# Optimization experiments

Measured on AMD Instinct MI355X. Metric: run time of the kernel, lower is better.

Reference implementation:

```python
import jax, jax.numpy as jnp
import numpy as np

B, L, D, H, WIN, EXP = 2, 4096, 1024, 16, 256, 4

def setup_inputs() -> dict:
    key = jax.random.key(0)
    ks = jax.random.split(key, 8)
    F = EXP * D
    p = lambda k, shape: jax.random.normal(k, shape, dtype=jnp.float32) * 0.02
    return {
        "x": jax.random.normal(ks[0], (B, L, D), dtype=jnp.float32),
        "mask": jnp.zeros((B, L), dtype=jnp.float32),  # 0 = local attention everywhere
        "Wq": p(ks[1], (D, D)), "bq": jnp.zeros((D,), jnp.float32),
        "Wk": p(ks[2], (D, D)), "bk": jnp.zeros((D,), jnp.float32),
        "Wv": p(ks[3], (D, D)), "bv": jnp.zeros((D,), jnp.float32),
        "ln_g": jnp.ones((D,), jnp.float32), "ln_b": jnp.zeros((D,), jnp.float32),
        "W1": p(ks[4], (D, F)), "b1": jnp.zeros((F,), jnp.float32),
        "W2": p(ks[5], (F, D)), "b2": jnp.zeros((D,), jnp.float32),
    }


def reference(x, mask, Wq, bq, Wk, bk, Wv, bv, ln_g, ln_b, W1, b1, W2, b2):
    NEG = jnp.asarray(-1e9, x.dtype)
    Bs, Ls, Ds = x.shape
    dh = Ds // H
    c = WIN // 2  # one-sided window size (HF uses attention_window // 2)
    pad = WIN - Ls % WIN
    xp = jnp.pad(x, ((0, 0), (0, pad), (0, 0)))  # pad_token_id == 0
    mp = jnp.pad(mask, ((0, 0), (0, pad)), constant_values=-10000.0)
    S = Ls + pad
    n = S // c  # number of query chunks of size c

    inv_sqrt_dh = jnp.asarray(1.0 / np.sqrt(dh), x.dtype)
    q = ((xp @ Wq + bq) * inv_sqrt_dh).reshape(Bs, S, H, dh)
    k = (xp @ Wk + bk).reshape(Bs, S, H, dh)
    v = (xp @ Wv + bv).reshape(Bs, S, H, dh)

    # pad keys/values by one chunk on each side so query chunk i sees chunks i-1,i,i+1
    kp = jnp.pad(k, ((0, 0), (c, c), (0, 0), (0, 0)))
    vp = jnp.pad(v, ((0, 0), (c, c), (0, 0), (0, 0)))
    kvalid = jnp.pad(mp == 0.0, ((0, 0), (c, c)), constant_values=False)  # [B, S+2c]

    idx = jnp.arange(n)[:, None] * c + jnp.arange(3 * c)[None, :]  # [n, 3c]
    kc = kp[:, idx]   # [B, n, 3c, H, dh]
    vc = vp[:, idx]   # [B, n, 3c, H, dh]
    kvc = kvalid[:, idx]  # [B, n, 3c]
    qc = q.reshape(Bs, n, c, H, dh)

    scores = jnp.einsum('bnphd,bnrhd->bhnpr', qc, kc)  # [B,H,n,c,3c]
    p_ = jnp.arange(c)[:, None]
    r_ = jnp.arange(3 * c)[None, :]
    band = (r_ >= p_) & (r_ <= p_ + 2 * c)  # exact |i-j| <= c band, [c,3c]
    valid = band[None, None, None, :, :] & kvc[:, None, :, None, :]
    scores = jnp.where(valid, scores, NEG)
    probs = jax.nn.softmax(scores, axis=-1)
    attn = jnp.einsum('bhnpr,bnrhd->bnphd', probs, vc).reshape(Bs, S, Ds)

    h = (xp + attn)[:, :Ls]  # residual then drop padding (matches module order)
    mu = jnp.mean(h, axis=-1, keepdims=True)
    var = jnp.var(h, axis=-1, keepdims=True)
    h = (h - mu) / jnp.sqrt(var + 1e-5) * ln_g + ln_b
    out = h + (jax.nn.gelu(h @ W1 + b1, approximate=False) @ W2 + b2)
    return out
```

## Files before the change

### kernel.cpp

```cpp
#include <hip/hip_runtime.h>
#include <hip/hip_bf16.h>
#include <cstdint>

typedef __attribute__((ext_vector_type(8))) short short8;
typedef __attribute__((ext_vector_type(4))) short short4v;
typedef __attribute__((ext_vector_type(4))) float floatx4;

constexpr int B_ = 2, L_ = 4096, D_ = 1024, H_ = 16, DH = 64, F_ = 4096;
constexpr int M_ = B_ * L_;
constexpr int NQKV = 3 * D_;
constexpr int VT_GUARD = 512;

constexpr size_t OFF_XB  = 0;
constexpr size_t OFF_WCT = OFF_XB  + (size_t)M_ * D_ * 2;
constexpr size_t OFF_W1T = OFF_WCT + (size_t)NQKV * D_ * 2;
constexpr size_t OFF_W2T = OFF_W1T + (size_t)F_ * D_ * 2;
constexpr size_t OFF_QKV = OFF_W2T + (size_t)D_ * F_ * 2;
constexpr size_t OFF_VT  = OFF_QKV + (size_t)M_ * NQKV * 2;
constexpr size_t OFF_ATT = OFF_VT  + ((size_t)B_*H_*DH*L_ + 2*VT_GUARD) * 2;
constexpr size_t OFF_HB  = OFF_ATT + (size_t)M_ * D_ * 2;
constexpr size_t OFF_MID = OFF_HB  + (size_t)M_ * D_ * 2;

static __device__ __forceinline__ float b2f(unsigned short u) {
    union { unsigned int i; float f; } v; v.i = ((unsigned int)u) << 16; return v.f;
}

static __device__ __forceinline__ void gload16(const void* g, void* l) {
    __builtin_amdgcn_global_load_lds(
        (const __attribute__((address_space(1))) uint32_t*)g,
        (__attribute__((address_space(3))) uint32_t*)l, 16, 0, 0);
}

__global__ __launch_bounds__(256) void k_cvt_x(const float* __restrict__ x,
                                               __hip_bfloat16* __restrict__ xb) {
    int i = (blockIdx.x * 256 + threadIdx.x) * 8;
    float4 a = *(const float4*)(x + i);
    float4 b = *(const float4*)(x + i + 4);
    alignas(16) __hip_bfloat16 t[8];
    t[0] = __float2bfloat16(a.x); t[1] = __float2bfloat16(a.y);
    t[2] = __float2bfloat16(a.z); t[3] = __float2bfloat16(a.w);
    t[4] = __float2bfloat16(b.x); t[5] = __float2bfloat16(b.y);
    t[6] = __float2bfloat16(b.z); t[7] = __float2bfloat16(b.w);
    *(uint4*)(xb + i) = *(const uint4*)t;
}

__global__ __launch_bounds__(256) void k_tcvt(const float* __restrict__ in,
                                              __hip_bfloat16* __restrict__ out,
                                              int R, int C) {
    __shared__ float t[64][65];
    int tx = threadIdx.x & 63, ty4 = threadIdx.x >> 6;
    int c0 = blockIdx.x * 64, r0 = blockIdx.y * 64;
#pragma unroll
    for (int i = 0; i < 16; i++) {
        int r = ty4 + i * 4;
        t[r][tx] = in[(size_t)(r0 + r) * C + c0 + tx];
    }
    __syncthreads();
#pragma unroll
    for (int i = 0; i < 16; i++) {
        int r = ty4 + i * 4;
        out[(size_t)(c0 + r) * R + r0 + tx] = __float2bfloat16(t[tx][r]);
    }
}

__global__ __launch_bounds__(256) void k_vtrans(const __hip_bfloat16* __restrict__ qkv,
                                                __hip_bfloat16* __restrict__ vtg) {
    __shared__ __hip_bfloat16 t[64][72];
    int tx = threadIdx.x & 63, ty4 = threadIdx.x >> 6;
    int bh = blockIdx.y, b = bh >> 4, h = bh & 15;
    int j0 = blockIdx.x * 64;
#pragma unroll
    for (int i = 0; i < 16; i++) {
        int j = ty4 + i * 4;
        t[j][tx] = qkv[(size_t)(b * L_ + j0 + j) * NQKV + 2 * D_ + h * DH + tx];
    }
    __syncthreads();
#pragma unroll
    for (int i = 0; i < 16; i++) {
        int d = ty4 + i * 4;
        vtg[(long)(bh * DH + d) * L_ + j0 + tx] = t[tx][d];
    }
}

template<int NBN, int GM, int EPI, int KTOT>
__global__ __launch_bounds__(256, 2)
void k_g2(const __hip_bfloat16* __restrict__ A, const __hip_bfloat16* __restrict__ BT,
          const float* __restrict__ b0p, const float* __restrict__ b1p,
          const float* __restrict__ b2p,
          __hip_bfloat16* __restrict__ obf, float* __restrict__ of32,
          const __hip_bfloat16* __restrict__ hres) {
    constexpr int KT = KTOT / 64;
    constexpr int NTOT = NBN * 128;
    constexpr int PER = GM * NBN;
    __shared__ __hip_bfloat16 As[2 * 2 * 128 * 32];
    __shared__ __hip_bfloat16 Bs[2 * 2 * 128 * 32];

    const int tid = threadIdx.x, wave = tid >> 6, lane = tid & 63;
    const int lo = lane & 15, hi = lane >> 4;
    const int wm = wave >> 1, wn = wave & 1;

    const int nwg = gridDim.x, q = nwg >> 3;
    const int bid = blockIdx.x;
    const int swz = (bid & 7) * q + (bid >> 3);
    const int g = swz / PER, r = swz % PER;
    const int bm = g * GM + (r % GM);
    const int bn = r / GM;
    const size_t m0 = (size_t)bm * 128, n0 = (size_t)bn * 128;

    const int chunkT = ((tid & 3) ^ ((tid >> 3) & 3)) * 8;
    const __hip_bfloat16* aG = A  + (m0 + (tid >> 2)) * (size_t)KTOT + chunkT;
    const __hip_bfloat16* bG = BT + (n0 + (tid >> 2)) * (size_t)KTOT + chunkT;
    const int ldsOff = wave * 512;

    const int swz16 = (hi ^ ((lo >> 1) & 3)) * 8;
    const int aOff = (wm * 64 + lo) * 32 + swz16;
    const int bOff = (wn * 64 + lo) * 32 + swz16;

    floatx4 acc[4][4] = {};

#define STAGE(buf, t)                                                         \
    _Pragma("unroll")                                                         \
    for (int kh = 0; kh < 2; ++kh)                                            \
        _Pragma("unroll")                                                     \
        for (int s = 0; s < 2; ++s) {                                         \
            gload16(aG + (size_t)(t) * 64 + kh * 32 + (size_t)s * 64 * KTOT,  \
                    As + (buf * 2 + kh) * 4096 + s * 2048 + ldsOff);          \
            gload16(bG + (size_t)(t) * 64 + kh * 32 + (size_t)s * 64 * KTOT,  \
                    Bs + (buf * 2 + kh) * 4096 + s * 2048 + ldsOff);          \
        }

    STAGE(0, 0)
    asm volatile("s_waitcnt vmcnt(0)" ::: "memory");
    __builtin_amdgcn_s_barrier();

    for (int t = 0; t < KT; ++t) {
        const int cur = t & 1;
        if (t + 1 < KT) {
            const int nxt = cur ^ 1;
            STAGE(nxt, t + 1)
        }
        const __hip_bfloat16* aU0 = As + (cur * 2 + 0) * 4096;
        const __hip_bfloat16* bU0 = Bs + (cur * 2 + 0) * 4096;
        const __hip_bfloat16* aU1 = As + (cur * 2 + 1) * 4096;
        const __hip_bfloat16* bU1 = Bs + (cur * 2 + 1) * 4096;
#pragma unroll
        for (int kh = 0; kh < 2; ++kh) {
            const __hip_bfloat16* aU = kh ? aU1 : aU0;
            const __hip_bfloat16* bU = kh ? bU1 : bU0;
            short8 afr[4], bfr[4];
#pragma unroll
            for (int i = 0; i < 4; ++i) {
                afr[i] = *(const short8*)(aU + aOff + i * 512);
                bfr[i] = *(const short8*)(bU + bOff + i * 512);
            }
#pragma unroll
            for (int mf = 0; mf < 4; ++mf)
#pragma unroll
                for (int nf = 0; nf < 4; ++nf)
                    acc[mf][nf] = __builtin_amdgcn_mfma_f32_16x16x32_bf16(
                        afr[mf], bfr[nf], acc[mf][nf], 0, 0, 0);
        }
        asm volatile("s_waitcnt vmcnt(0)" ::: "memory");
        __builtin_amdgcn_sched_barrier(0);
        __builtin_amdgcn_s_barrier();
    }
#undef STAGE

#pragma unroll
    for (int mf = 0; mf < 4; ++mf) {
        const int row = (int)m0 + wm * 64 + mf * 16 + hi * 4;
#pragma unroll
        for (int nf = 0; nf < 4; ++nf) {
            const int col = (int)n0 + wn * 64 + nf * 16 + lo;
#pragma unroll
            for (int rr = 0; rr < 4; ++rr) {
                float v = acc[mf][nf][rr];
                const size_t ro = (size_t)(row + rr);
                if (EPI == 0) {
                    float bia = (col < 1024) ? b0p[col]
                              : (col < 2048 ? b1p[col - 1024] : b2p[col - 2048]);
                    obf[ro * NQKV + col] = __float2bfloat16(v + bia);
                } else if (EPI == 1) {
                    v += b0p[col];
                    v = 0.5f * v * (1.0f + erff(v * 0.70710678118654752440f));
                    obf[ro * F_ + col] = __float2bfloat16(v);
                } else {
                    v += b0p[col];
                    v += b2f(*(const unsigned short*)&hres[ro * D_ + col]);
                    of32[ro * D_ + col] = v;
                }
            }
        }
    }
    (void)NTOT;
}

__global__ __launch_bounds__(256, 2)
void k_attn(const __hip_bfloat16* __restrict__ qkv, const float* __restrict__ mask,
            const __hip_bfloat16* __restrict__ vtg, __hip_bfloat16* __restrict__ attnb) {
    constexpr int PS = 296;
    __shared__ __hip_bfloat16 P[4][16 * PS];
    const int tid = threadIdx.x, wave = tid >> 6, lane = tid & 63;
    const int bh = blockIdx.y, b = bh >> 4, h = bh & 15;
    const int q0 = blockIdx.x * 64 + wave * 16;
    const int lo = lane & 15, hi = lane >> 4;

    short8 qf0, qf1;
    {
        const __hip_bfloat16* qb = qkv + (size_t)(b * L_ + q0 + lo) * NQKV + h * DH + hi * 8;
        qf0 = *(const short8*)qb;
        qf1 = *(const short8*)(qb + 32);
    }

    floatx4 sc[17];
    const __hip_bfloat16* kcol = qkv + (size_t)b * L_ * NQKV + D_ + h * DH + hi * 8;
#pragma unroll
    for (int t = 0; t < 17; t++) {
        int jg = q0 - 128 + t * 16 + lo;
        int jc = jg < 0 ? 0 : (jg >= L_ ? L_ - 1 : jg);
        const __hip_bfloat16* kb = kcol + (size_t)jc * NQKV;
        short8 kf0 = *(const short8*)kb;
        short8 kf1 = *(const short8*)(kb + 32);
        floatx4 a = {};
        a = __builtin_amdgcn_mfma_f32_16x16x32_bf16(qf0, kf0, a, 0, 0, 0);
        a = __builtin_amdgcn_mfma_f32_16x16x32_bf16(qf1, kf1, a, 0, 0, 0);
        float mval = mask[b * L_ + jc];
        bool jok = (jg >= 0) && (jg < L_) && (mval == 0.0f);
#pragma unroll
        for (int r = 0; r < 4; r++) {
            int qi = q0 + hi * 4 + r;
            bool ok = jok && (jg >= qi - 128) && (jg <= qi + 128);
            a[r] = ok ? a[r] * 0.125f : -1e9f;
        }
        sc[t] = a;
    }

#pragma unroll
    for (int r = 0; r < 4; r++) {
        float m = -3e38f;
#pragma unroll
        for (int t = 0; t < 17; t++) m = fmaxf(m, sc[t][r]);
        m = fmaxf(m, __shfl_xor(m, 1));
        m = fmaxf(m, __shfl_xor(m, 2));
        m = fmaxf(m, __shfl_xor(m, 4));
        m = fmaxf(m, __shfl_xor(m, 8));
        float s = 0.0f;
#pragma unroll
        for (int t = 0; t < 17; t++) { float e = __expf(sc[t][r] - m); sc[t][r] = e; s += e; }
        s += __shfl_xor(s, 1); s += __shfl_xor(s, 2);
        s += __shfl_xor(s, 4); s += __shfl_xor(s, 8);
        float inv = 1.0f / s;
#pragma unroll
        for (int t = 0; t < 17; t++) sc[t][r] *= inv;
    }

    __hip_bfloat16* Pw = &P[wave][0];
#pragma unroll
    for (int t = 0; t < 17; t++)
#pragma unroll
        for (int r = 0; r < 4; r++)
            Pw[(hi * 4 + r) * PS + t * 16 + lo] = __float2bfloat16(sc[t][r]);
    {
        int zr = lane >> 2, zc = 272 + (lane & 3) * 4;
        __hip_bfloat16 z = __float2bfloat16(0.0f);
#pragma unroll
        for (int i = 0; i < 4; i++) Pw[zr * PS + zc + i] = z;
    }

    floatx4 o[4] = {};
#pragma unroll
    for (int st = 0; st < 9; st++) {
        short8 pa = *(const short8*)(Pw + lo * PS + st * 32 + hi * 8);
        int jb = q0 - 128 + st * 32 + hi * 8;
#pragma unroll
        for (int dt = 0; dt < 4; dt++) {
            const __hip_bfloat16* vb = vtg + (long)(bh * DH + dt * 16 + lo) * L_ + jb;
            short8 vf = *(const short8*)vb;
            o[dt] = __builtin_amdgcn_mfma_f32_16x16x32_bf16(pa, vf, o[dt], 0, 0, 0);
        }
    }

#pragma unroll
    for (int dt = 0; dt < 4; dt++)
#pragma unroll
        for (int r = 0; r < 4; r++) {
            int row = q0 + hi * 4 + r;
            attnb[(size_t)(b * L_ + row) * D_ + h * DH + dt * 16 + lo] =
                __float2bfloat16(o[dt][r]);
        }
}

__global__ __launch_bounds__(256)
void k_ln(const float* __restrict__ x, const __hip_bfloat16* __restrict__ attnb,
          const float* __restrict__ g, const float* __restrict__ bt,
          __hip_bfloat16* __restrict__ hb) {
    const int row = blockIdx.x, tid = threadIdx.x;
    const int c4 = tid * 4;
    float4 xv = *(const float4*)(x + (size_t)row * D_ + c4);
    short4v av = *(const short4v*)(attnb + (size_t)row * D_ + c4);
    float h0 = xv.x + b2f((unsigned short)av[0]);
    float h1 = xv.y + b2f((unsigned short)av[1]);
    float h2 = xv.z + b2f((unsigned short)av[2]);
    float h3 = xv.w + b2f((unsigned short)av[3]);
    float s = h0 + h1 + h2 + h3;
    float q = h0 * h0 + h1 * h1 + h2 * h2 + h3 * h3;
#pragma unroll
    for (int off = 32; off > 0; off >>= 1) {
        s += __shfl_down(s, off);
        q += __shfl_down(q, off);
    }
    __shared__ float red[8];
    int wave = tid >> 6, lane = tid & 63;
    if (lane == 0) { red[wave] = s; red[4 + wave] = q; }
    __syncthreads();
    s = red[0] + red[1] + red[2] + red[3];
    q = red[4] + red[5] + red[6] + red[7];
    float mu = s * (1.0f / D_);
    float var = q * (1.0f / D_) - mu * mu;
    float inv = rsqrtf(var + 1e-5f);
    float4 gv = *(const float4*)(g + c4);
    float4 bv = *(const float4*)(bt + c4);
    alignas(8) __hip_bfloat16 ov[4];
    ov[0] = __float2bfloat16((h0 - mu) * inv * gv.x + bv.x);
    ov[1] = __float2bfloat16((h1 - mu) * inv * gv.y + bv.y);
    ov[2] = __float2bfloat16((h2 - mu) * inv * gv.z + bv.z);
    ov[3] = __float2bfloat16((h3 - mu) * inv * gv.w + bv.w);
    *(short4v*)(hb + (size_t)row * D_ + c4) = *(const short4v*)ov;
}

extern "C" void kernel_launch(void* const* d_in, const int* in_sizes, int n_in,
                              void* d_out, int out_size, void* d_ws, size_t ws_size,
                              hipStream_t stream) {
    const float* x    = (const float*)d_in[0];
    const float* mask = (const float*)d_in[1];
    const float* Wq   = (const float*)d_in[2];
    const float* bq   = (const float*)d_in[3];
    const float* Wk   = (const float*)d_in[4];
    const float* bk   = (const float*)d_in[5];
    const float* Wv   = (const float*)d_in[6];
    const float* bv   = (const float*)d_in[7];
    const float* ln_g = (const float*)d_in[8];
    const float* ln_b = (const float*)d_in[9];
    const float* W1   = (const float*)d_in[10];
    const float* b1   = (const float*)d_in[11];
    const float* W2   = (const float*)d_in[12];
    const float* b2   = (const float*)d_in[13];
    float* out = (float*)d_out;
    char* ws = (char*)d_ws;

    __hip_bfloat16* xb   = (__hip_bfloat16*)(ws + OFF_XB);
    __hip_bfloat16* wct  = (__hip_bfloat16*)(ws + OFF_WCT);
    __hip_bfloat16* w1t  = (__hip_bfloat16*)(ws + OFF_W1T);
    __hip_bfloat16* w2t  = (__hip_bfloat16*)(ws + OFF_W2T);
    __hip_bfloat16* qkvb = (__hip_bfloat16*)(ws + OFF_QKV);
    __hip_bfloat16* vtg  = (__hip_bfloat16*)(ws + OFF_VT) + VT_GUARD;
    __hip_bfloat16* attb = (__hip_bfloat16*)(ws + OFF_ATT);
    __hip_bfloat16* hb   = (__hip_bfloat16*)(ws + OFF_HB);
    __hip_bfloat16* midb = (__hip_bfloat16*)(ws + OFF_MID);

    k_cvt_x<<<(M_ * D_) / 2048, 256, 0, stream>>>(x, xb);
    k_tcvt<<<dim3(D_ / 64, D_ / 64), 256, 0, stream>>>(Wq, wct,                   D_, D_);
    k_tcvt<<<dim3(D_ / 64, D_ / 64), 256, 0, stream>>>(Wk, wct + 1024 * 1024,     D_, D_);
    k_tcvt<<<dim3(D_ / 64, D_ / 64), 256, 0, stream>>>(Wv, wct + 2 * 1024 * 1024, D_, D_);
    k_tcvt<<<dim3(F_ / 64, D_ / 64), 256, 0, stream>>>(W1, w1t, D_, F_);
    k_tcvt<<<dim3(D_ / 64, F_ / 64), 256, 0, stream>>>(W2, w2t, F_, D_);

    k_g2<24, 8, 0, D_><<<64 * 24, 256, 0, stream>>>(
        xb, wct, bq, bk, bv, qkvb, nullptr, nullptr);

    k_vtrans<<<dim3(L_ / 64, B_ * H_), 256, 0, stream>>>(qkvb, vtg);
    k_attn<<<dim3(L_ / 64, B_ * H_), 256, 0, stream>>>(qkvb, mask, vtg, attb);

    k_ln<<<M_, 256, 0, stream>>>(x, attb, ln_g, ln_b, hb);

    k_g2<32, 8, 1, D_><<<64 * 32, 256, 0, stream>>>(
        hb, w1t, b1, nullptr, nullptr, midb, nullptr, nullptr);
    k_g2<8, 2, 2, F_><<<64 * 8, 256, 0, stream>>>(
        midb, w2t, b2, nullptr, nullptr, nullptr, out, hb);
}
```

Before: 549.5 us.

## Replace GEMM kernel with 8-wave 256-row tiles and interleaved load/MFMA schedule

Swaps the 4-wave 128x128 GEMM for an 8-wave kernel with 256-row tiles and 128- or 256-column tiles, using a 64-wide K stage with an XOR-swizzled LDS layout. Each K step is split into four phases: the prefetch loads for the next stage are interleaved with fragment reads and MFMA bursts, with partial vmcnt waits and s_setprio raised around the MFMA bursts. The goal is more reuse per tile and better overlap of global loads with matrix math. The cost is more LDS, more accumulator registers, many more barriers per K step, and fewer workgroups for the smaller GEMMs.

```diff
diff --git a/kernel.cpp b/kernel.cpp
--- a/kernel.cpp
+++ b/kernel.cpp
@@ -82,22 +82,23 @@
     }
 }
 
-template<int NBN, int GM, int EPI, int KTOT>
-__global__ __launch_bounds__(256, 2)
-void k_g2(const __hip_bfloat16* __restrict__ A, const __hip_bfloat16* __restrict__ BT,
+template<int NFRAG, int GM, int EPI, int KTOT, int NBN>
+__global__ __launch_bounds__(512, 2)
+void k_g8(const __hip_bfloat16* __restrict__ A, const __hip_bfloat16* __restrict__ BT,
           const float* __restrict__ b0p, const float* __restrict__ b1p,
           const float* __restrict__ b2p,
           __hip_bfloat16* __restrict__ obf, float* __restrict__ of32,
           const __hip_bfloat16* __restrict__ hres) {
+    constexpr int BN = NFRAG * 64;
     constexpr int KT = KTOT / 64;
-    constexpr int NTOT = NBN * 128;
     constexpr int PER = GM * NBN;
-    __shared__ __hip_bfloat16 As[2 * 2 * 128 * 32];
-    __shared__ __hip_bfloat16 Bs[2 * 2 * 128 * 32];
+
+    __shared__ __hip_bfloat16 AS[2][4 * 4096];
+    __shared__ __hip_bfloat16 BS[2][NFRAG * 4096];
 
     const int tid = threadIdx.x, wave = tid >> 6, lane = tid & 63;
     const int lo = lane & 15, hi = lane >> 4;
-    const int wm = wave >> 1, wn = wave & 1;
+    const int wm = wave >> 2, wn = wave & 3;
 
     const int nwg = gridDim.x, q = nwg >> 3;
     const int bid = blockIdx.x;
@@ -105,76 +106,137 @@
     const int g = swz / PER, r = swz % PER;
     const int bm = g * GM + (r % GM);
     const int bn = r / GM;
-    const size_t m0 = (size_t)bm * 128, n0 = (size_t)bn * 128;
-
-    const int chunkT = ((tid & 3) ^ ((tid >> 3) & 3)) * 8;
-    const __hip_bfloat16* aG = A  + (m0 + (tid >> 2)) * (size_t)KTOT + chunkT;
-    const __hip_bfloat16* bG = BT + (n0 + (tid >> 2)) * (size_t)KTOT + chunkT;
-    const int ldsOff = wave * 512;
-
-    const int swz16 = (hi ^ ((lo >> 1) & 3)) * 8;
-    const int aOff = (wm * 64 + lo) * 32 + swz16;
-    const int bOff = (wn * 64 + lo) * 32 + swz16;
-
-    floatx4 acc[4][4] = {};
-
-#define STAGE(buf, t)                                                         \
-    _Pragma("unroll")                                                         \
-    for (int kh = 0; kh < 2; ++kh)                                            \
-        _Pragma("unroll")                                                     \
-        for (int s = 0; s < 2; ++s) {                                         \
-            gload16(aG + (size_t)(t) * 64 + kh * 32 + (size_t)s * 64 * KTOT,  \
-                    As + (buf * 2 + kh) * 4096 + s * 2048 + ldsOff);          \
-            gload16(bG + (size_t)(t) * 64 + kh * 32 + (size_t)s * 64 * KTOT,  \
-                    Bs + (buf * 2 + kh) * 4096 + s * 2048 + ldsOff);          \
-        }
-
-    STAGE(0, 0)
+    const size_t m0 = (size_t)bm * 256, n0 = (size_t)bn * BN;
+
+    const int srow = tid >> 3;
+    const int gcc = (tid & 7) ^ (srow & 7);
+    const __hip_bfloat16* aG = A  + (m0 + srow) * (size_t)KTOT + gcc * 8;
+    const __hip_bfloat16* bG = BT + (n0 + srow) * (size_t)KTOT + gcc * 8;
+    const int ldst = wave * 512;
+
+    int ccr[2];
+#pragma unroll
+    for (int k = 0; k < 2; ++k) ccr[k] = ((k * 4 + hi) ^ (lo & 7)) * 8;
+    const int Ra = wm * 128 + lo;
+    const int Rb0 = wn * (NFRAG * 16) + lo;
+
+    floatx4 acc[8][NFRAG] = {};
+
+#define STG_A(buf, sw, tn) gload16(aG + (size_t)(sw) * 64 * KTOT + (size_t)(tn) * 64, \
+                                   &AS[buf][(sw) * 4096 + ldst])
+#define STG_B(buf, sw, tn) gload16(bG + (size_t)(sw) * 64 * KTOT + (size_t)(tn) * 64, \
+                                   &BS[buf][(sw) * 4096 + ldst])
+
+    STG_B(0, 0, 0); STG_B(0, 1, 0);
+    if (NFRAG == 4) { STG_B(0, 2, 0); STG_B(0, 3, 0); }
+    STG_A(0, 0, 0); STG_A(0, 2, 0); STG_A(0, 1, 0); STG_A(0, 3, 0);
     asm volatile("s_waitcnt vmcnt(0)" ::: "memory");
     __builtin_amdgcn_s_barrier();
 
     for (int t = 0; t < KT; ++t) {
-        const int cur = t & 1;
-        if (t + 1 < KT) {
-            const int nxt = cur ^ 1;
-            STAGE(nxt, t + 1)
-        }
-        const __hip_bfloat16* aU0 = As + (cur * 2 + 0) * 4096;
-        const __hip_bfloat16* bU0 = Bs + (cur * 2 + 0) * 4096;
-        const __hip_bfloat16* aU1 = As + (cur * 2 + 1) * 4096;
-        const __hip_bfloat16* bU1 = Bs + (cur * 2 + 1) * 4096;
-#pragma unroll
-        for (int kh = 0; kh < 2; ++kh) {
-            const __hip_bfloat16* aU = kh ? aU1 : aU0;
-            const __hip_bfloat16* bU = kh ? bU1 : bU0;
-            short8 afr[4], bfr[4];
-#pragma unroll
-            for (int i = 0; i < 4; ++i) {
-                afr[i] = *(const short8*)(aU + aOff + i * 512);
-                bfr[i] = *(const short8*)(bU + bOff + i * 512);
-            }
-#pragma unroll
-            for (int mf = 0; mf < 4; ++mf)
-#pragma unroll
-                for (int nf = 0; nf < 4; ++nf)
-                    acc[mf][nf] = __builtin_amdgcn_mfma_f32_16x16x32_bf16(
-                        afr[mf], bfr[nf], acc[mf][nf], 0, 0, 0);
-        }
-        asm volatile("s_waitcnt vmcnt(0)" ::: "memory");
-        __builtin_amdgcn_sched_barrier(0);
-        __builtin_amdgcn_s_barrier();
-    }
-#undef STAGE
-
-#pragma unroll
-    for (int mf = 0; mf < 4; ++mf) {
-        const int row = (int)m0 + wm * 64 + mf * 16 + hi * 4;
-#pragma unroll
-        for (int nf = 0; nf < 4; ++nf) {
-            const int col = (int)n0 + wn * 64 + nf * 16 + lo;
+        const int cur = t & 1, nxt = cur ^ 1;
+        const int tn = (t + 1 < KT) ? (t + 1) : 0;
+        const __hip_bfloat16* aL = &AS[cur][0];
+        const __hip_bfloat16* bL = &BS[cur][0];
+        short8 bfr[NFRAG][2], afr[2][2];
+
+#pragma unroll
+        for (int gf = 0; gf < NFRAG; ++gf)
+#pragma unroll
+            for (int k = 0; k < 2; ++k)
+                bfr[gf][k] = *(const short8*)(bL + (Rb0 + gf * 16) * 64 + ccr[k]);
+#pragma unroll
+        for (int f = 0; f < 2; ++f)
+#pragma unroll
+            for (int k = 0; k < 2; ++k)
+                afr[f][k] = *(const short8*)(aL + (Ra + f * 16) * 64 + ccr[k]);
+        STG_B(nxt, 0, tn); STG_B(nxt, 1, tn);
+        __builtin_amdgcn_s_barrier();
+        __builtin_amdgcn_s_setprio(1);
+#pragma unroll
+        for (int f = 0; f < 2; ++f)
+#pragma unroll
+            for (int gf = 0; gf < NFRAG; ++gf)
+#pragma unroll
+                for (int k = 0; k < 2; ++k)
+                    acc[f][gf] = __builtin_amdgcn_mfma_f32_16x16x32_bf16(
+                        afr[f][k], bfr[gf][k], acc[f][gf], 0, 0, 0);
+        __builtin_amdgcn_s_setprio(0);
+        __builtin_amdgcn_s_barrier();
+
+#pragma unroll
+        for (int f = 0; f < 2; ++f)
+#pragma unroll
+            for (int k = 0; k < 2; ++k)
+                afr[f][k] = *(const short8*)(aL + (Ra + (2 + f) * 16) * 64 + ccr[k]);
+        if (NFRAG == 4) { STG_B(nxt, 2, tn); STG_B(nxt, 3, tn); }
+        else            { STG_A(nxt, 0, tn); STG_A(nxt, 2, tn); }
+        asm volatile("s_waitcnt vmcnt(4)" ::: "memory");
+        __builtin_amdgcn_s_barrier();
+        __builtin_amdgcn_s_setprio(1);
+#pragma unroll
+        for (int f = 0; f < 2; ++f)
+#pragma unroll
+            for (int gf = 0; gf < NFRAG; ++gf)
+#pragma unroll
+                for (int k = 0; k < 2; ++k)
+                    acc[2 + f][gf] = __builtin_amdgcn_mfma_f32_16x16x32_bf16(
+                        afr[f][k], bfr[gf][k], acc[2 + f][gf], 0, 0, 0);
+        __builtin_amdgcn_s_setprio(0);
+        __builtin_amdgcn_s_barrier();
+
+#pragma unroll
+        for (int f = 0; f < 2; ++f)
+#pragma unroll
+            for (int k = 0; k < 2; ++k)
+                afr[f][k] = *(const short8*)(aL + (Ra + (4 + f) * 16) * 64 + ccr[k]);
+        if (NFRAG == 4) { STG_A(nxt, 0, tn); STG_A(nxt, 2, tn); }
+        else            { STG_A(nxt, 1, tn); STG_A(nxt, 3, tn); }
+        __builtin_amdgcn_s_barrier();
+        __builtin_amdgcn_s_setprio(1);
+#pragma unroll
+        for (int f = 0; f < 2; ++f)
+#pragma unroll
+            for (int gf = 0; gf < NFRAG; ++gf)
+#pragma unroll
+                for (int k = 0; k < 2; ++k)
+                    acc[4 + f][gf] = __builtin_amdgcn_mfma_f32_16x16x32_bf16(
+                        afr[f][k], bfr[gf][k], acc[4 + f][gf], 0, 0, 0);
+        __builtin_amdgcn_s_setprio(0);
+        __builtin_amdgcn_s_barrier();
+
+#pragma unroll
+        for (int f = 0; f < 2; ++f)
+#pragma unroll
+            for (int k = 0; k < 2; ++k)
+                afr[f][k] = *(const short8*)(aL + (Ra + (6 + f) * 16) * 64 + ccr[k]);
+        if (NFRAG == 4) { STG_A(nxt, 1, tn); STG_A(nxt, 3, tn); }
+        asm volatile("s_waitcnt vmcnt(2)" ::: "memory");
+        __builtin_amdgcn_s_barrier();
+        __builtin_amdgcn_s_setprio(1);
+#pragma unroll
+        for (int f = 0; f < 2; ++f)
+#pragma unroll
+            for (int gf = 0; gf < NFRAG; ++gf)
+#pragma unroll
+                for (int k = 0; k < 2; ++k)
+                    acc[6 + f][gf] = __builtin_amdgcn_mfma_f32_16x16x32_bf16(
+                        afr[f][k], bfr[gf][k], acc[6 + f][gf], 0, 0, 0);
+        __builtin_amdgcn_s_setprio(0);
+        __builtin_amdgcn_s_barrier();
+    }
+#undef STG_A
+#undef STG_B
+
+#pragma unroll
+    for (int mf = 0; mf < 8; ++mf) {
+        const int row = (int)m0 + wm * 128 + mf * 16 + hi * 4;
+#pragma unroll
+        for (int gf = 0; gf < NFRAG; ++gf) {
+            const int col = (int)n0 + wn * (NFRAG * 16) + gf * 16 + lo;
 #pragma unroll
             for (int rr = 0; rr < 4; ++rr) {
-                float v = acc[mf][nf][rr];
+                float v = acc[mf][gf][rr];
                 const size_t ro = (size_t)(row + rr);
                 if (EPI == 0) {
                     float bia = (col < 1024) ? b0p[col]
@@ -192,7 +254,6 @@
             }
         }
     }
-    (void)NTOT;
 }
 
 __global__ __launch_bounds__(256, 2)
@@ -365,7 +426,7 @@
     k_tcvt<<<dim3(F_ / 64, D_ / 64), 256, 0, stream>>>(W1, w1t, D_, F_);
     k_tcvt<<<dim3(D_ / 64, F_ / 64), 256, 0, stream>>>(W2, w2t, F_, D_);
 
-    k_g2<24, 8, 0, D_><<<64 * 24, 256, 0, stream>>>(
+    k_g8<2, 4, 0, D_, 24><<<768, 512, 0, stream>>>(
         xb, wct, bq, bk, bv, qkvb, nullptr, nullptr);
 
     k_vtrans<<<dim3(L_ / 64, B_ * H_), 256, 0, stream>>>(qkvb, vtg);
@@ -373,8 +434,8 @@
 
     k_ln<<<M_, 256, 0, stream>>>(x, attb, ln_g, ln_b, hb);
 
-    k_g2<32, 8, 1, D_><<<64 * 32, 256, 0, stream>>>(
+    k_g8<4, 4, 1, D_, 16><<<512, 512, 0, stream>>>(
         hb, w1t, b1, nullptr, nullptr, midb, nullptr, nullptr);
-    k_g2<8, 2, 2, F_><<<64 * 8, 256, 0, stream>>>(
+    k_g8<2, 4, 2, F_, 8><<<256, 512, 0, stream>>>(
         midb, w2t, b2, nullptr, nullptr, nullptr, out, hb);
 }
```

Measured after the change: 505.4 us. -8.0%, faster.

## Rewrite GEMM kernel with triple-buffered K=32 pipeline and wider 512-thread tiles

Applied to the files above, without the earlier changes.

Replaces the double-buffered K=64 GEMM with a three-stage LDS ring of K=32 slices, prefetching two steps ahead and waiting on a partial vmcnt so global loads overlap compute. The QKV and W1 GEMMs move to 512-thread blocks with 128x256 tiles, which halves the grid. The LDS swizzle is also changed, and MFMA sections are wrapped in s_setprio. The aim is to hide global-load latency and improve operand reuse, at the cost of higher LDS and register use per block and possibly fewer resident blocks.

```diff
diff --git a/kernel.cpp b/kernel.cpp
--- a/kernel.cpp
+++ b/kernel.cpp
@@ -82,22 +82,27 @@
     }
 }
 
-template<int NBN, int GM, int EPI, int KTOT>
-__global__ __launch_bounds__(256, 2)
-void k_g2(const __hip_bfloat16* __restrict__ A, const __hip_bfloat16* __restrict__ BT,
+template<int NT, int WN, int GM, int EPI, int KTOT, int NBN, int MINW>
+__global__ __launch_bounds__(NT, MINW)
+void k_p3(const __hip_bfloat16* __restrict__ A, const __hip_bfloat16* __restrict__ BT,
           const float* __restrict__ b0p, const float* __restrict__ b1p,
           const float* __restrict__ b2p,
           __hip_bfloat16* __restrict__ obf, float* __restrict__ of32,
           const __hip_bfloat16* __restrict__ hres) {
-    constexpr int KT = KTOT / 64;
-    constexpr int NTOT = NBN * 128;
+    constexpr int BN = WN * 64;
+    constexpr int KT = KTOT / 32;
     constexpr int PER = GM * NBN;
-    __shared__ __hip_bfloat16 As[2 * 2 * 128 * 32];
-    __shared__ __hip_bfloat16 Bs[2 * 2 * 128 * 32];
+    constexpr int A_LOADS = (128 * 4) / NT;
+    constexpr int B_LOADS = (BN * 4) / NT;
+    constexpr int LPT = A_LOADS + B_LOADS;
+    constexpr int RSWEEP = NT / 4;
+
+    __shared__ __hip_bfloat16 AS[3][128 * 32];
+    __shared__ __hip_bfloat16 BS[3][BN * 32];
 
     const int tid = threadIdx.x, wave = tid >> 6, lane = tid & 63;
     const int lo = lane & 15, hi = lane >> 4;
-    const int wm = wave >> 1, wn = wave & 1;
+    const int wm = wave / WN, wn = wave % WN;
 
     const int nwg = gridDim.x, q = nwg >> 3;
     const int bid = blockIdx.x;
@@ -105,66 +110,74 @@
     const int g = swz / PER, r = swz % PER;
     const int bm = g * GM + (r % GM);
     const int bn = r / GM;
-    const size_t m0 = (size_t)bm * 128, n0 = (size_t)bn * 128;
-
-    const int chunkT = ((tid & 3) ^ ((tid >> 3) & 3)) * 8;
-    const __hip_bfloat16* aG = A  + (m0 + (tid >> 2)) * (size_t)KTOT + chunkT;
-    const __hip_bfloat16* bG = BT + (n0 + (tid >> 2)) * (size_t)KTOT + chunkT;
-    const int ldsOff = wave * 512;
-
-    const int swz16 = (hi ^ ((lo >> 1) & 3)) * 8;
-    const int aOff = (wm * 64 + lo) * 32 + swz16;
-    const int bOff = (wn * 64 + lo) * 32 + swz16;
+    const size_t m0 = (size_t)bm * 128, n0 = (size_t)bn * BN;
+
+    const int r0 = tid >> 2;
+    const int gcc = (tid & 3) ^ (r0 & 3);
+    const __hip_bfloat16* aG = A  + (m0 + r0) * (size_t)KTOT + gcc * 8;
+    const __hip_bfloat16* bG = BT + (n0 + r0) * (size_t)KTOT + gcc * 8;
+
+    const int cR = (hi ^ (lo & 3)) * 8;
+    const int aOff = (wm * 64 + lo) * 32 + cR;
+    const int bOff = (wn * 64 + lo) * 32 + cR;
 
     floatx4 acc[4][4] = {};
 
-#define STAGE(buf, t)                                                         \
-    _Pragma("unroll")                                                         \
-    for (int kh = 0; kh < 2; ++kh)                                            \
+#define STAGE(buf, kt)                                                        \
+    do {                                                                      \
         _Pragma("unroll")                                                     \
-        for (int s = 0; s < 2; ++s) {                                         \
-            gload16(aG + (size_t)(t) * 64 + kh * 32 + (size_t)s * 64 * KTOT,  \
-                    As + (buf * 2 + kh) * 4096 + s * 2048 + ldsOff);          \
-            gload16(bG + (size_t)(t) * 64 + kh * 32 + (size_t)s * 64 * KTOT,  \
-                    Bs + (buf * 2 + kh) * 4096 + s * 2048 + ldsOff);          \
-        }
-
-    STAGE(0, 0)
-    asm volatile("s_waitcnt vmcnt(0)" ::: "memory");
+        for (int s = 0; s < A_LOADS; ++s)                                     \
+            gload16(aG + (size_t)(s * RSWEEP) * KTOT + (size_t)(kt) * 32,     \
+                    &AS[buf][(s * NT + wave * 64) * 8]);                      \
+        _Pragma("unroll")                                                     \
+        for (int s = 0; s < B_LOADS; ++s)                                     \
+            gload16(bG + (size_t)(s * RSWEEP) * KTOT + (size_t)(kt) * 32,     \
+                    &BS[buf][(s * NT + wave * 64) * 8]);                      \
+    } while (0)
+
+#define WAITVM_LPT()                                                          \
+    do {                                                                      \
+        if constexpr (LPT == 3) asm volatile("s_waitcnt vmcnt(3)" ::: "memory"); \
+        else                    asm volatile("s_waitcnt vmcnt(4)" ::: "memory"); \
+    } while (0)
+
+    STAGE(0, 0);
+    STAGE(1, 1);
+    WAITVM_LPT();
+    __builtin_amdgcn_sched_barrier(0);
     __builtin_amdgcn_s_barrier();
 
+    int cur = 0, nb = 2;
     for (int t = 0; t < KT; ++t) {
-        const int cur = t & 1;
-        if (t + 1 < KT) {
-            const int nxt = cur ^ 1;
-            STAGE(nxt, t + 1)
-        }
-        const __hip_bfloat16* aU0 = As + (cur * 2 + 0) * 4096;
-        const __hip_bfloat16* bU0 = Bs + (cur * 2 + 0) * 4096;
-        const __hip_bfloat16* aU1 = As + (cur * 2 + 1) * 4096;
-        const __hip_bfloat16* bU1 = Bs + (cur * 2 + 1) * 4096;
-#pragma unroll
-        for (int kh = 0; kh < 2; ++kh) {
-            const __hip_bfloat16* aU = kh ? aU1 : aU0;
-            const __hip_bfloat16* bU = kh ? bU1 : bU0;
-            short8 afr[4], bfr[4];
-#pragma unroll
-            for (int i = 0; i < 4; ++i) {
-                afr[i] = *(const short8*)(aU + aOff + i * 512);
-                bfr[i] = *(const short8*)(bU + bOff + i * 512);
-            }
-#pragma unroll
-            for (int mf = 0; mf < 4; ++mf)
-#pragma unroll
-                for (int nf = 0; nf < 4; ++nf)
-                    acc[mf][nf] = __builtin_amdgcn_mfma_f32_16x16x32_bf16(
-                        afr[mf], bfr[nf], acc[mf][nf], 0, 0, 0);
-        }
-        asm volatile("s_waitcnt vmcnt(0)" ::: "memory");
+        const int tf = (t + 2 < KT) ? (t + 2) : t;
+        STAGE(nb, tf);
+
+        const __hip_bfloat16* aL = &AS[cur][0];
+        const __hip_bfloat16* bL = &BS[cur][0];
+        short8 afr[4], bfr[4];
+#pragma unroll
+        for (int f = 0; f < 4; ++f) afr[f] = *(const short8*)(aL + aOff + f * 512);
+#pragma unroll
+        for (int f = 0; f < 4; ++f) bfr[f] = *(const short8*)(bL + bOff + f * 512);
+
+        __builtin_amdgcn_s_setprio(1);
+#pragma unroll
+        for (int mf = 0; mf < 4; ++mf)
+#pragma unroll
+            for (int nf = 0; nf < 4; ++nf)
+                acc[mf][nf] = __builtin_amdgcn_mfma_f32_16x16x32_bf16(
+                    afr[mf], bfr[nf], acc[mf][nf], 0, 0, 0);
+        __builtin_amdgcn_s_setprio(0);
+
+        WAITVM_LPT();
         __builtin_amdgcn_sched_barrier(0);
         __builtin_amdgcn_s_barrier();
+
+        cur = (cur == 2) ? 0 : cur + 1;
+        nb  = (nb  == 2) ? 0 : nb  + 1;
     }
 #undef STAGE
+#undef WAITVM_LPT
 
 #pragma unroll
     for (int mf = 0; mf < 4; ++mf) {
@@ -192,7 +205,6 @@
             }
         }
     }
-    (void)NTOT;
 }
 
 __global__ __launch_bounds__(256, 2)
@@ -365,7 +377,7 @@
     k_tcvt<<<dim3(F_ / 64, D_ / 64), 256, 0, stream>>>(W1, w1t, D_, F_);
     k_tcvt<<<dim3(D_ / 64, F_ / 64), 256, 0, stream>>>(W2, w2t, F_, D_);
 
-    k_g2<24, 8, 0, D_><<<64 * 24, 256, 0, stream>>>(
+    k_p3<512, 4, 8, 0, D_, 12, 4><<<768, 512, 0, stream>>>(
         xb, wct, bq, bk, bv, qkvb, nullptr, nullptr);
 
     k_vtrans<<<dim3(L_ / 64, B_ * H_), 256, 0, stream>>>(qkvb, vtg);
@@ -373,8 +385,8 @@
 
     k_ln<<<M_, 256, 0, stream>>>(x, attb, ln_g, ln_b, hb);
 
-    k_g2<32, 8, 1, D_><<<64 * 32, 256, 0, stream>>>(
+    k_p3<512, 4, 8, 1, D_, 16, 4><<<1024, 512, 0, stream>>>(
         hb, w1t, b1, nullptr, nullptr, midb, nullptr, nullptr);
-    k_g2<8, 2, 2, F_><<<64 * 8, 256, 0, stream>>>(
+    k_p3<256, 2, 2, 2, F_, 8, 3><<<512, 256, 0, stream>>>(
         midb, w2t, b2, nullptr, nullptr, nullptr, out, hb);
 }
```

Result: faster. 490.3 us (-10.8%).
